# Kernel optimization log

Measured on AMD Instinct MI355X. Metric: run time of the kernel, lower is better.

The kernel has to match this reference:

```python
import jax, jax.numpy as jnp
import numpy as np

MIN_NORM = 1e-15
EPS = 1e-5
C_CURV = 1.0  # args.c

def _norm(x):
    return jnp.clip(jnp.linalg.norm(x, axis=-1, keepdims=True), MIN_NORM)

def artanh(x):
    x = jnp.clip(x, -1.0 + EPS, 1.0 - EPS)
    return 0.5 * (jnp.log1p(x) - jnp.log1p(-x))

def proj(x, c):
    # clip points to stay strictly inside the Poincare ball
    norm = _norm(x)
    maxnorm = (1.0 - EPS) / jnp.sqrt(c)
    return jnp.where(norm > maxnorm, x / norm * maxnorm, x)

def expmap0(u, c):
    sqrt_c = jnp.sqrt(c)
    u_norm = _norm(u)
    return jnp.tanh(sqrt_c * u_norm) * u / (sqrt_c * u_norm)

def logmap0(p, c):
    sqrt_c = jnp.sqrt(c)
    p_norm = _norm(p)
    return artanh(sqrt_c * p_norm) * p / (sqrt_c * p_norm)

def mobius_add(x, y, c):
    x2 = jnp.sum(x * x, axis=-1, keepdims=True)
    y2 = jnp.sum(y * y, axis=-1, keepdims=True)
    xy = jnp.sum(x * y, axis=-1, keepdims=True)
    num = (1.0 + 2.0 * c * xy + c * y2) * x + (1.0 - c * x2) * y
    denom = 1.0 + 2.0 * c * xy + c * c * x2 * y2
    return num / jnp.clip(denom, MIN_NORM)

def mobius_matvec(W, x, c):
    sqrt_c = jnp.sqrt(c)
    x_norm = _norm(x)
    mx = x @ W.T
    mx_norm = _norm(mx)
    return jnp.tanh(mx_norm / x_norm * artanh(sqrt_c * x_norm)) * mx / (mx_norm * sqrt_c)

def poincare_dist(x, y, c):
    sqrt_c = jnp.sqrt(c)
    d = _norm(mobius_add(-x, y, c))[..., 0]
    return 2.0 / sqrt_c * artanh(sqrt_c * d)

def hgnn_layer(h, adj, W, b, c):
    # HypLinear: mobius matvec + hyperbolic bias
    mv = proj(mobius_matvec(W, h, c), c)
    hyp_b = proj(expmap0(b, c), c)
    h = proj(mobius_add(mv, hyp_b, c), c)
    # HypAgg: aggregate in tangent space at origin
    h = proj(expmap0(adj @ logmap0(h, c), c), c)
    # HypAct: relu in tangent space
    return proj(expmap0(jax.nn.relu(logmap0(h, c)), c), c)

def setup_inputs() -> dict:
    key = jax.random.key(0)
    ks = jax.random.split(key, 10)
    N, D, C, NC, NODE_C, L = 8192, 128, 64, 7, 7, 4
    x = jax.random.normal(ks[0], (N, D), jnp.float32)
    adj = jax.random.uniform(ks[1], (N, N), jnp.float32) / N  # row-stochastic-ish dense adjacency
    graph_indicator = jax.random.randint(ks[2], (N,), 0, 1)
    W_conv = jax.random.normal(ks[3], (L, D, D), jnp.float32) / np.sqrt(D)
    b_conv = jax.random.normal(ks[4], (L, D), jnp.float32) * 0.01
    centroids = jax.random.normal(ks[5], (C, D), jnp.float32) * 0.1
    W_mlp = jax.random.normal(ks[6], (NC, C), jnp.float32) * 0.1
    b_mlp = jnp.zeros((NC,), jnp.float32)
    W_mlp1 = jax.random.normal(ks[7], (NODE_C, D), jnp.float32) * 0.1
    b_mlp1 = jnp.zeros((NODE_C,), jnp.float32)
    return {"x": x, "adj": adj, "graph_indicator": graph_indicator,
            "W_conv": W_conv, "b_conv": b_conv, "centroids": centroids,
            "W_mlp": W_mlp, "b_mlp": b_mlp, "W_mlp1": W_mlp1, "b_mlp1": b_mlp1}

def reference(x, adj, graph_indicator, W_conv, b_conv, centroids, W_mlp, b_mlp, W_mlp1, b_mlp1):
    c = C_CURV
    # proj_tan0 is identity for PoincareBall
    h = proj(expmap0(x, c), c)
    # 2 residual blocks, each with 2 HGNN layers; shortcut is identity (in_dim == out_dim)
    for blk in range(2):
        res = h
        for j in range(2):
            idx = blk * 2 + j
            h = hgnn_layer(h, adj, W_conv[idx], b_conv[idx], c)
        h = h + res  # Euclidean residual, as in the source
    # CentroidDistance: pairwise hyperbolic distance [N, C]
    node_centroid_dist = poincare_dist(h[:, None, :], centroids[None, :, :], c)
    readout = jnp.mean(node_centroid_dist, axis=0, keepdims=True)  # [1, C]
    h_r = logmap0(readout, c)  # proj_tan0(logmap0(.)) -> identity proj_tan0
    logits = jax.nn.softmax(h_r @ W_mlp.T + b_mlp, axis=0)[None]        # [1,1,NC]
    h1 = logmap0(h, c)
    logits_node = jax.nn.softmax(h1 @ W_mlp1.T + b_mlp1, axis=0)[None]  # [1,N,node_classes]
    return (logits, logits_node, h_r)
```

## Files before the change

### kernel.cpp

```cpp
#include <hip/hip_runtime.h>

#define MIN_NORM 1e-15f
#define EPSV 1e-5f
#define MAXN (1.0f - EPSV)
#define NN 8192
#define DD 128

typedef unsigned short u16;
typedef __bf16 bf16x8 __attribute__((ext_vector_type(8)));
typedef float f32x4 __attribute__((ext_vector_type(4)));

__device__ __forceinline__ float wave_sum(float v) {
#pragma unroll
  for (int off = 32; off > 0; off >>= 1) v += __shfl_xor(v, off, 64);
  return v;
}

__device__ __forceinline__ float artanh_f(float x) {
  x = fminf(fmaxf(x, -1.0f + EPSV), 1.0f - EPSV);
  return 0.5f * (log1pf(x) - log1pf(-x));
}

__device__ __forceinline__ u16 f2bf(float f) {
  unsigned u = __float_as_uint(f);
  unsigned r = (u + 0x7fffu + ((u >> 16) & 1u)) >> 16;
  return (u16)r;
}
__device__ __forceinline__ float bf2f(u16 b) { return __uint_as_float(((unsigned)b) << 16); }

template <bool AF32>
__global__ __launch_bounds__(256) void gemm_bt(const void* __restrict__ Av,
                                               const u16* __restrict__ Bt,
                                               float* __restrict__ Cp,
                                               int M, int K, int KC) {
  __shared__ __align__(16) float As[64 * 68];
  __shared__ __align__(16) u16 Bs[128 * 72];
  u16* Ash = (u16*)As;

  const int tid = threadIdx.x;
  const int lane = tid & 63;
  const int w = tid >> 6;
  const int wm = w >> 1, wn = w & 1;
  const int lrow = lane & 15;
  const int lq = lane >> 4;
  const int m0 = blockIdx.x * 64;
  const int kk0 = blockIdx.y * KC;

  f32x4 acc[2][4];
#pragma unroll
  for (int a = 0; a < 2; a++)
#pragma unroll
    for (int b = 0; b < 4; b++)
#pragma unroll
      for (int r = 0; r < 4; r++) acc[a][b][r] = 0.0f;

  for (int kt = 0; kt < KC; kt += 64) {
    const int kk = kk0 + kt;
    __syncthreads();
    if constexpr (AF32) {
      const float* A = (const float*)Av;
#pragma unroll
      for (int it = 0; it < 4; it++) {
        int idx = it * 256 + tid;
        int r = idx >> 4, c = (idx & 15) << 2;
        float4 v = *(const float4*)(A + (size_t)(m0 + r) * K + kk + c);
        *(float4*)&As[r * 68 + c] = v;
      }
    } else {
      const u16* A = (const u16*)Av;
#pragma unroll
      for (int it = 0; it < 2; it++) {
        int idx = it * 256 + tid;
        int r = idx >> 3, c = (idx & 7) << 3;
        uint4 v = *(const uint4*)(A + (size_t)(m0 + r) * K + kk + c);
        *(uint4*)&Ash[r * 72 + c] = v;
      }
    }
#pragma unroll
    for (int it = 0; it < 4; it++) {
      int idx = it * 256 + tid;
      int n = idx >> 3, c = (idx & 7) << 3;
      uint4 v = *(const uint4*)(Bt + (size_t)n * K + kk + c);
      *(uint4*)&Bs[n * 72 + c] = v;
    }
    __syncthreads();
#pragma unroll
    for (int ks = 0; ks < 2; ks++) {
      const int kloc = ks * 32 + lq * 8;
      bf16x8 af[2], bfr[4];
#pragma unroll
      for (int ti = 0; ti < 2; ti++) {
        int r = wm * 32 + ti * 16 + lrow;
        if constexpr (AF32) {
          const float* p = &As[r * 68 + kloc];
          float4 q0 = *(const float4*)p;
          float4 q1 = *(const float4*)(p + 4);
          bf16x8 t;
          t[0] = (__bf16)q0.x; t[1] = (__bf16)q0.y; t[2] = (__bf16)q0.z; t[3] = (__bf16)q0.w;
          t[4] = (__bf16)q1.x; t[5] = (__bf16)q1.y; t[6] = (__bf16)q1.z; t[7] = (__bf16)q1.w;
          af[ti] = t;
        } else {
          af[ti] = *(const bf16x8*)&Ash[r * 72 + kloc];
        }
      }
#pragma unroll
      for (int tj = 0; tj < 4; tj++) {
        int n = wn * 64 + tj * 16 + lrow;
        bfr[tj] = *(const bf16x8*)&Bs[n * 72 + kloc];
      }
#pragma unroll
      for (int ti = 0; ti < 2; ti++)
#pragma unroll
        for (int tj = 0; tj < 4; tj++)
          acc[ti][tj] = __builtin_amdgcn_mfma_f32_16x16x32_bf16(af[ti], bfr[tj], acc[ti][tj], 0, 0, 0);
    }
  }
  float* C = Cp + (size_t)blockIdx.y * M * 128;
#pragma unroll
  for (int ti = 0; ti < 2; ti++)
#pragma unroll
    for (int tj = 0; tj < 4; tj++)
#pragma unroll
      for (int r = 0; r < 4; r++) {
        int row = m0 + wm * 32 + ti * 16 + lq * 4 + r;
        int col = wn * 64 + tj * 16 + lrow;
        C[(size_t)row * 128 + col] = acc[ti][tj][r];
      }
}

__global__ void build_wt(const float* __restrict__ W, u16* __restrict__ Wt2) {
  int idx = blockIdx.x * 256 + threadIdx.x;
  if (idx >= 4 * 128 * 128) return;
  int layer = idx >> 14;
  int n = (idx >> 7) & 127;
  int k = idx & 127;
  float e = W[idx];
  u16 hi = f2bf(e);
  u16 lo = f2bf(e - bf2f(hi));
  u16* base = Wt2 + (size_t)layer * 128 * 384 + (size_t)n * 384;
  base[k] = hi;
  base[128 + k] = hi;
  base[256 + k] = lo;
}

__device__ __forceinline__ void write_split(u16* hs, int i, int lane, float v0, float v1) {
  u16* row = hs + (size_t)i * 384;
  u16 h0 = f2bf(v0), h1 = f2bf(v1);
  u16 l0 = f2bf(v0 - bf2f(h0)), l1 = f2bf(v1 - bf2f(h1));
  row[lane] = h0;         row[lane + 64] = h1;
  row[128 + lane] = l0;   row[128 + 64 + lane] = l1;
  row[256 + lane] = h0;   row[256 + 64 + lane] = h1;
}

__global__ __launch_bounds__(64) void rowwise_init(const float* __restrict__ x,
                                                   float* __restrict__ h,
                                                   float* __restrict__ res,
                                                   u16* __restrict__ hsplit) {
  int i = blockIdx.x, lane = threadIdx.x;
  const float* xr = x + (size_t)i * DD;
  float a0 = xr[lane], a1 = xr[lane + 64];
  float n = fmaxf(sqrtf(wave_sum(a0 * a0 + a1 * a1)), MIN_NORM);
  float g = tanhf(n) / n;
  float y0 = g * a0, y1 = g * a1;
  float pn = fmaxf(sqrtf(wave_sum(y0 * y0 + y1 * y1)), MIN_NORM);
  float s = pn > MAXN ? MAXN / pn : 1.0f;
  y0 *= s; y1 *= s;
  size_t base = (size_t)i * DD;
  h[base + lane] = y0;   h[base + lane + 64] = y1;
  res[base + lane] = y0; res[base + lane + 64] = y1;
  write_split(hsplit, i, lane, y0, y1);
}

__global__ __launch_bounds__(64) void rowwise_mid(const float* __restrict__ h,
                                                  const float* __restrict__ mx,
                                                  const float* __restrict__ bvec,
                                                  u16* __restrict__ uT) {
  int i = blockIdx.x, lane = threadIdx.x;
  const float* hr = h + (size_t)i * DD;
  const float* mr = mx + (size_t)i * DD;
  float h0 = hr[lane], h1 = hr[lane + 64];
  float m0 = mr[lane], m1 = mr[lane + 64];
  float xn = fmaxf(sqrtf(wave_sum(h0 * h0 + h1 * h1)), MIN_NORM);
  float mn = fmaxf(sqrtf(wave_sum(m0 * m0 + m1 * m1)), MIN_NORM);
  float t = tanhf(mn / xn * artanh_f(xn));
  float v0 = t * m0 / mn, v1 = t * m1 / mn;
  float pn = fmaxf(sqrtf(wave_sum(v0 * v0 + v1 * v1)), MIN_NORM);
  float sc = pn > MAXN ? MAXN / pn : 1.0f;
  v0 *= sc; v1 *= sc;
  float b0 = bvec[lane], b1 = bvec[lane + 64];
  float bn = fmaxf(sqrtf(wave_sum(b0 * b0 + b1 * b1)), MIN_NORM);
  float gb = tanhf(bn) / bn;
  float e0 = gb * b0, e1 = gb * b1;
  float en = fmaxf(sqrtf(wave_sum(e0 * e0 + e1 * e1)), MIN_NORM);
  float sb = en > MAXN ? MAXN / en : 1.0f;
  e0 *= sb; e1 *= sb;
  float x2 = wave_sum(v0 * v0 + v1 * v1);
  float y2 = wave_sum(e0 * e0 + e1 * e1);
  float xy = wave_sum(v0 * e0 + v1 * e1);
  float ca = 1.0f + 2.0f * xy + y2;
  float cb = 1.0f - x2;
  float den = fmaxf(1.0f + 2.0f * xy + x2 * y2, MIN_NORM);
  float t0 = (ca * v0 + cb * e0) / den, t1 = (ca * v1 + cb * e1) / den;
  float tn = fmaxf(sqrtf(wave_sum(t0 * t0 + t1 * t1)), MIN_NORM);
  float st = tn > MAXN ? MAXN / tn : 1.0f;
  t0 *= st; t1 *= st;
  float pn2 = fmaxf(sqrtf(wave_sum(t0 * t0 + t1 * t1)), MIN_NORM);
  float gl = artanh_f(pn2) / pn2;
  uT[(size_t)lane * NN + i] = f2bf(gl * t0);
  uT[(size_t)(lane + 64) * NN + i] = f2bf(gl * t1);
}

__global__ __launch_bounds__(64) void rowwise_post(const float* __restrict__ P,
                                                   float* __restrict__ h,
                                                   float* __restrict__ res,
                                                   u16* __restrict__ hsplit,
                                                   int addres) {
  int i = blockIdx.x, lane = threadIdx.x;
  size_t base = (size_t)i * DD;
  float m0 = 0.f, m1 = 0.f;
#pragma unroll
  for (int sk = 0; sk < 4; sk++) {
    const float* p = P + (size_t)sk * NN * DD + base;
    m0 += p[lane];
    m1 += p[lane + 64];
  }
  float n = fmaxf(sqrtf(wave_sum(m0 * m0 + m1 * m1)), MIN_NORM);
  float g = tanhf(n) / n;
  float y0 = g * m0, y1 = g * m1;
  float pn = fmaxf(sqrtf(wave_sum(y0 * y0 + y1 * y1)), MIN_NORM);
  float s = pn > MAXN ? MAXN / pn : 1.0f;
  y0 *= s; y1 *= s;
  float hn = fmaxf(sqrtf(wave_sum(y0 * y0 + y1 * y1)), MIN_NORM);
  float gl = artanh_f(hn) / hn;
  float u0 = fmaxf(gl * y0, 0.0f), u1 = fmaxf(gl * y1, 0.0f);
  float un = fmaxf(sqrtf(wave_sum(u0 * u0 + u1 * u1)), MIN_NORM);
  float ge = tanhf(un) / un;
  float z0 = ge * u0, z1 = ge * u1;
  float zn = fmaxf(sqrtf(wave_sum(z0 * z0 + z1 * z1)), MIN_NORM);
  float sz = zn > MAXN ? MAXN / zn : 1.0f;
  z0 *= sz; z1 *= sz;
  if (addres) {
    z0 += res[base + lane];
    z1 += res[base + lane + 64];
    res[base + lane] = z0;
    res[base + lane + 64] = z1;
  }
  h[base + lane] = z0;
  h[base + lane + 64] = z1;
  write_split(hsplit, i, lane, z0, z1);
}

__global__ __launch_bounds__(256) void centroid_k(const float* __restrict__ h,
                                                  const float* __restrict__ cen,
                                                  float* __restrict__ rs) {
  __shared__ float cs[64 * 129];
  __shared__ float hs[32 * 128];
  __shared__ float y2s[64];
  int tid = threadIdx.x;
  int i0 = blockIdx.x * 32;
  for (int idx = tid; idx < 64 * 128; idx += 256) {
    int r = idx >> 7, c = idx & 127;
    cs[r * 129 + c] = cen[idx];
  }
  for (int idx = tid; idx < 32 * 128; idx += 256) hs[idx] = h[(size_t)i0 * 128 + idx];
  __syncthreads();
  if (tid < 64) {
    float s = 0.f;
    for (int k = 0; k < 128; k++) { float v = cs[tid * 129 + k]; s = fmaf(v, v, s); }
    y2s[tid] = s;
  }
  __syncthreads();
  int w = tid >> 6, lane = tid & 63;
  float dsum = 0.f;
  for (int rr = 0; rr < 8; rr++) {
    int r = w * 8 + rr;
    float dot = 0.f, x2 = 0.f;
    for (int k = 0; k < 128; k++) {
      float hk = hs[r * 128 + k];
      dot = fmaf(hk, cs[lane * 129 + k], dot);
      x2 = fmaf(hk, hk, x2);
    }
    float y2 = y2s[lane];
    float al = 1.0f - 2.0f * dot + y2;
    float be = 1.0f - x2;
    float num2 = al * al * x2 + be * be * y2 - 2.0f * al * be * dot;
    float den = fmaxf(1.0f - 2.0f * dot + x2 * y2, MIN_NORM);
    float d = fmaxf(sqrtf(fmaxf(num2, 0.0f)) / den, MIN_NORM);
    dsum += 2.0f * artanh_f(d);
  }
  atomicAdd(&rs[lane], dsum);
}

__global__ __launch_bounds__(64) void finalize_k(const float* __restrict__ rs,
                                                 float* __restrict__ out) {
  int lane = threadIdx.x;
  float r = rs[lane] * (1.0f / 8192.0f);
  float n = fmaxf(sqrtf(wave_sum(r * r)), MIN_NORM);
  float a = artanh_f(n);
  out[7 + NN * 7 + lane] = a * r / n;
  if (lane < 7) out[lane] = 1.0f;
}

__global__ __launch_bounds__(64) void scores_k(const float* __restrict__ h,
                                               const float* __restrict__ Wm,
                                               const float* __restrict__ bm,
                                               float* __restrict__ sc) {
  int i = blockIdx.x, lane = threadIdx.x;
  const float* hr = h + (size_t)i * DD;
  float h0 = hr[lane], h1 = hr[lane + 64];
  float pn = fmaxf(sqrtf(wave_sum(h0 * h0 + h1 * h1)), MIN_NORM);
  float gl = artanh_f(pn) / pn;
  float u0 = gl * h0, u1 = gl * h1;
  float p[7];
#pragma unroll
  for (int j = 0; j < 7; j++)
    p[j] = wave_sum(u0 * Wm[j * 128 + lane] + u1 * Wm[j * 128 + lane + 64]);
  float v = p[0];
#pragma unroll
  for (int j = 1; j < 7; j++)
    if (lane == j) v = p[j];
  if (lane < 7) sc[(size_t)i * 7 + lane] = v + bm[lane];
}

__global__ __launch_bounds__(256) void softmax_col(const float* __restrict__ sc,
                                                   float* __restrict__ out) {
  __shared__ float buf[256][8];
  int tid = threadIdx.x;
  float mx[7];
#pragma unroll
  for (int j = 0; j < 7; j++) mx[j] = -1e30f;
  for (int i = tid; i < NN; i += 256)
#pragma unroll
    for (int j = 0; j < 7; j++) mx[j] = fmaxf(mx[j], sc[i * 7 + j]);
#pragma unroll
  for (int j = 0; j < 7; j++) buf[tid][j] = mx[j];
  __syncthreads();
  for (int off = 128; off > 0; off >>= 1) {
    if (tid < off)
#pragma unroll
      for (int j = 0; j < 7; j++) buf[tid][j] = fmaxf(buf[tid][j], buf[tid + off][j]);
    __syncthreads();
  }
  float cm[7];
#pragma unroll
  for (int j = 0; j < 7; j++) cm[j] = buf[0][j];
  __syncthreads();
  float sm[7];
#pragma unroll
  for (int j = 0; j < 7; j++) sm[j] = 0.f;
  for (int i = tid; i < NN; i += 256)
#pragma unroll
    for (int j = 0; j < 7; j++) sm[j] += expf(sc[i * 7 + j] - cm[j]);
#pragma unroll
  for (int j = 0; j < 7; j++) buf[tid][j] = sm[j];
  __syncthreads();
  for (int off = 128; off > 0; off >>= 1) {
    if (tid < off)
#pragma unroll
      for (int j = 0; j < 7; j++) buf[tid][j] += buf[tid + off][j];
    __syncthreads();
  }
  float csum[7];
#pragma unroll
  for (int j = 0; j < 7; j++) csum[j] = buf[0][j];
  __syncthreads();
  for (int idx = tid; idx < NN * 7; idx += 256) {
    int i = idx / 7, j = idx - i * 7;
    out[idx] = expf(sc[i * 7 + j] - cm[j]) / csum[j];
  }
}

extern "C" void kernel_launch(void* const* d_in, const int* in_sizes, int n_in,
                              void* d_out, int out_size, void* d_ws, size_t ws_size,
                              hipStream_t stream) {
  const float* x = (const float*)d_in[0];
  const float* adj = (const float*)d_in[1];
  const float* W_conv = (const float*)d_in[3];
  const float* b_conv = (const float*)d_in[4];
  const float* centroids = (const float*)d_in[5];
  const float* W_mlp1 = (const float*)d_in[8];
  const float* b_mlp1 = (const float*)d_in[9];
  float* out = (float*)d_out;

  char* ws = (char*)d_ws;
  size_t off = 0;
  auto alloc = [&](size_t bytes) {
    void* p = ws + off;
    off = (off + bytes + 255) & ~(size_t)255;
    return p;
  };
  float* h = (float*)alloc((size_t)NN * DD * 4);
  float* res = (float*)alloc((size_t)NN * DD * 4);
  u16* hsplit = (u16*)alloc((size_t)NN * 384 * 2);
  u16* uT = (u16*)alloc((size_t)DD * NN * 2);
  u16* Wt2 = (u16*)alloc((size_t)4 * 128 * 384 * 2);
  float* P = (float*)alloc((size_t)4 * NN * DD * 4);
  float* scores = (float*)alloc((size_t)NN * 7 * 4);
  float* rs = (float*)alloc(64 * 4);
  (void)ws_size; (void)in_sizes; (void)n_in; (void)out_size;

  hipMemsetAsync(rs, 0, 64 * 4, stream);
  build_wt<<<(4 * 128 * 128 + 255) / 256, 256, 0, stream>>>(W_conv, Wt2);
  rowwise_init<<<NN, 64, 0, stream>>>(x, h, res, hsplit);
  for (int layer = 0; layer < 4; layer++) {
    gemm_bt<false><<<dim3(NN / 64, 1), 256, 0, stream>>>(
        hsplit, Wt2 + (size_t)layer * 128 * 384, P, NN, 384, 384);
    rowwise_mid<<<NN, 64, 0, stream>>>(h, P, b_conv + layer * DD, uT);
    gemm_bt<true><<<dim3(NN / 64, 4), 256, 0, stream>>>(
        adj, uT, P, NN, NN, NN / 4);
    rowwise_post<<<NN, 64, 0, stream>>>(P, h, res, hsplit, (layer & 1));
  }
  centroid_k<<<256, 256, 0, stream>>>(h, centroids, rs);
  finalize_k<<<1, 64, 0, stream>>>(rs, out);
  scores_k<<<NN, 64, 0, stream>>>(h, W_mlp1, b_mlp1, scores);
  softmax_col<<<1, 256, 0, stream>>>(scores, out + 7);
}
```

Baseline: 971.4 us.

## Cache bf16 copy of adjacency in first layer and raise split-K

The first adjacency GEMM now writes a bf16 copy of the fp32 adjacency while it streams it, and the later three layers read that bf16 copy instead of the fp32 matrix. This halves the adjacency bytes read in those layers, but the first layer pays extra writes. The split-K factor rises from 4 to 8 for the adjacency GEMM and from 1 to 3 for the weight GEMM, so the row-wise kernels now sum more partial buffers. The A shared-memory buffer is sized per template so the bf16 path uses less LDS.

```diff
diff --git a/kernel.cpp b/kernel.cpp
--- a/kernel.cpp
+++ b/kernel.cpp
@@ -28,14 +28,17 @@
 }
 __device__ __forceinline__ float bf2f(u16 b) { return __uint_as_float(((unsigned)b) << 16); }
 
-template <bool AF32>
+template <bool AF32, bool DUMP>
 __global__ __launch_bounds__(256) void gemm_bt(const void* __restrict__ Av,
                                                const u16* __restrict__ Bt,
                                                float* __restrict__ Cp,
+                                               u16* __restrict__ Adump,
                                                int M, int K, int KC) {
-  __shared__ __align__(16) float As[64 * 68];
+  constexpr int ABYTES = AF32 ? (64 * 68 * 4) : (64 * 72 * 2);
+  __shared__ __align__(16) char Abuf[ABYTES];
   __shared__ __align__(16) u16 Bs[128 * 72];
-  u16* Ash = (u16*)As;
+  float* As = (float*)Abuf;
+  u16* Ash = (u16*)Abuf;
 
   const int tid = threadIdx.x;
   const int lane = tid & 63;
@@ -65,6 +68,11 @@
         int r = idx >> 4, c = (idx & 15) << 2;
         float4 v = *(const float4*)(A + (size_t)(m0 + r) * K + kk + c);
         *(float4*)&As[r * 68 + c] = v;
+        if constexpr (DUMP) {
+          ushort4 d;
+          d.x = f2bf(v.x); d.y = f2bf(v.y); d.z = f2bf(v.z); d.w = f2bf(v.w);
+          *(ushort4*)(Adump + (size_t)(m0 + r) * K + kk + c) = d;
+        }
       }
     } else {
       const u16* A = (const u16*)Av;
@@ -172,14 +180,20 @@
 }
 
 __global__ __launch_bounds__(64) void rowwise_mid(const float* __restrict__ h,
-                                                  const float* __restrict__ mx,
+                                                  const float* __restrict__ P,
                                                   const float* __restrict__ bvec,
                                                   u16* __restrict__ uT) {
   int i = blockIdx.x, lane = threadIdx.x;
-  const float* hr = h + (size_t)i * DD;
-  const float* mr = mx + (size_t)i * DD;
+  size_t base = (size_t)i * DD;
+  const float* hr = h + base;
   float h0 = hr[lane], h1 = hr[lane + 64];
-  float m0 = mr[lane], m1 = mr[lane + 64];
+  float m0 = 0.f, m1 = 0.f;
+#pragma unroll
+  for (int sk = 0; sk < 3; sk++) {
+    const float* p = P + (size_t)sk * NN * DD + base;
+    m0 += p[lane];
+    m1 += p[lane + 64];
+  }
   float xn = fmaxf(sqrtf(wave_sum(h0 * h0 + h1 * h1)), MIN_NORM);
   float mn = fmaxf(sqrtf(wave_sum(m0 * m0 + m1 * m1)), MIN_NORM);
   float t = tanhf(mn / xn * artanh_f(xn));
@@ -219,7 +233,7 @@
   size_t base = (size_t)i * DD;
   float m0 = 0.f, m1 = 0.f;
 #pragma unroll
-  for (int sk = 0; sk < 4; sk++) {
+  for (int sk = 0; sk < 8; sk++) {
     const float* p = P + (size_t)sk * NN * DD + base;
     m0 += p[lane];
     m1 += p[lane + 64];
@@ -394,7 +408,8 @@
   u16* hsplit = (u16*)alloc((size_t)NN * 384 * 2);
   u16* uT = (u16*)alloc((size_t)DD * NN * 2);
   u16* Wt2 = (u16*)alloc((size_t)4 * 128 * 384 * 2);
-  float* P = (float*)alloc((size_t)4 * NN * DD * 4);
+  float* P = (float*)alloc((size_t)8 * NN * DD * 4);
+  u16* adjbf = (u16*)alloc((size_t)NN * NN * 2);
   float* scores = (float*)alloc((size_t)NN * 7 * 4);
   float* rs = (float*)alloc(64 * 4);
   (void)ws_size; (void)in_sizes; (void)n_in; (void)out_size;
@@ -403,11 +418,16 @@
   build_wt<<<(4 * 128 * 128 + 255) / 256, 256, 0, stream>>>(W_conv, Wt2);
   rowwise_init<<<NN, 64, 0, stream>>>(x, h, res, hsplit);
   for (int layer = 0; layer < 4; layer++) {
-    gemm_bt<false><<<dim3(NN / 64, 1), 256, 0, stream>>>(
-        hsplit, Wt2 + (size_t)layer * 128 * 384, P, NN, 384, 384);
+    gemm_bt<false, false><<<dim3(NN / 64, 3), 256, 0, stream>>>(
+        hsplit, Wt2 + (size_t)layer * 128 * 384, P, nullptr, NN, 384, 128);
     rowwise_mid<<<NN, 64, 0, stream>>>(h, P, b_conv + layer * DD, uT);
-    gemm_bt<true><<<dim3(NN / 64, 4), 256, 0, stream>>>(
-        adj, uT, P, NN, NN, NN / 4);
+    if (layer == 0) {
+      gemm_bt<true, true><<<dim3(NN / 64, 8), 256, 0, stream>>>(
+          adj, uT, P, adjbf, NN, NN, NN / 8);
+    } else {
+      gemm_bt<false, false><<<dim3(NN / 64, 8), 256, 0, stream>>>(
+          adjbf, uT, P, nullptr, NN, NN, NN / 8);
+    }
     rowwise_post<<<NN, 64, 0, stream>>>(P, h, res, hsplit, (layer & 1));
   }
   centroid_k<<<256, 256, 0, stream>>>(h, centroids, rs);
```

Result: faster. 873.6 us (-10.1%).
